# Kernel tuning notes

Measured on AMD Instinct MI355X. Metric: run time of the kernel, lower is better.

Reference implementation:

```python
import jax, jax.numpy as jnp
import numpy as np

N = 6144
INPUT_SIZE = 1024
HIDDEN = 256
NEG_INF = -9e15  # matches torch masked_fill value -9000000000000000.0


def setup_inputs() -> dict:
    key = jax.random.key(0)
    k1, k2, k3, k4 = jax.random.split(key, 4)
    nodes_embed = jax.random.normal(k1, (N, INPUT_SIZE), dtype=jnp.float32)
    node_adj = jax.random.randint(k2, (N, N), 0, 2, dtype=jnp.int32)
    # learned params (xavier-uniform-ish scaling)
    limW = np.sqrt(6.0 / (INPUT_SIZE + HIDDEN))
    W = jax.random.uniform(k3, (INPUT_SIZE, HIDDEN), minval=-limW, maxval=limW, dtype=jnp.float32)
    lima = 1.414 * np.sqrt(6.0 / (2 * HIDDEN + 1))
    a_edge = jax.random.uniform(k4, (2 * HIDDEN,), minval=-lima, maxval=lima, dtype=jnp.float32)
    return {"nodes_embed": nodes_embed, "W": W, "a_edge": a_edge, "node_adj": node_adj}


def reference(nodes_embed, W, a_edge, node_adj):
    # h = nodes_embed @ W : [N, hidden]
    h = nodes_embed @ W
    # W_edge([h_i ; h_j]) decomposes exactly: (h_i @ a1) + (h_j @ a2)
    a1, a2 = a_edge[:HIDDEN], a_edge[HIDDEN:]
    score = (h @ a1)[:, None] + (h @ a2)[None, :]  # [N, N]
    adj_f = node_adj.astype(h.dtype)
    weight = jax.nn.leaky_relu(adj_f * score, negative_slope=0.2)
    weight = jnp.where(node_adj == 0, jnp.asarray(NEG_INF, h.dtype), weight)
    attention = jax.nn.softmax(weight, axis=-1)
    # dropout in eval mode (identity)
    return attention @ h  # [N, hidden]
```

## Files before the change

kernel.cpp:

```cpp
#include <hip/hip_runtime.h>
#include <hip/hip_bf16.h>

#define NN 6144
#define INPUT 1024
#define HID 256

using frag  = __attribute__((ext_vector_type(8))) short;
using f32x4 = __attribute__((ext_vector_type(4))) float;

static __device__ __forceinline__ unsigned short bf16u(float x) {
    unsigned u = __float_as_uint(x);
    u += 0x7fff + ((u >> 16) & 1);
    return (unsigned short)(u >> 16);
}

static __device__ __forceinline__ void gll16nt(const void* g, void* l) {
    __builtin_amdgcn_global_load_lds((__attribute__((address_space(1))) const void*)g,
                                     (__attribute__((address_space(3))) void*)l, 16, 0, 2);
}

static __device__ __forceinline__ void lds_barrier() {
    asm volatile("s_waitcnt lgkmcnt(0)" ::: "memory");
    __builtin_amdgcn_s_barrier();
    __builtin_amdgcn_sched_barrier(0);
}


__global__ __launch_bounds__(256) void k_prep(const float* __restrict__ X,
                                              const float* __restrict__ W,
                                              unsigned short* __restrict__ Xbp,
                                              unsigned short* __restrict__ Wtp) {
    int b = blockIdx.x;
    if (b < 3072) {
        int t = b * 256 + threadIdx.x;
        int i = t >> 7, k8 = t & 127;
        const float4* p = reinterpret_cast<const float4*>(X + (size_t)i * INPUT + k8 * 8);
        float4 x0 = p[0], x1 = p[1];
        frag v;
        v[0] = (short)bf16u(x0.x); v[1] = (short)bf16u(x0.y);
        v[2] = (short)bf16u(x0.z); v[3] = (short)bf16u(x0.w);
        v[4] = (short)bf16u(x1.x); v[5] = (short)bf16u(x1.y);
        v[6] = (short)bf16u(x1.z); v[7] = (short)bf16u(x1.w);
        size_t off = ((size_t)((i >> 4) * 32 + (k8 >> 2))) * 512 + (k8 & 3) * 128 + (i & 15) * 8;
        *reinterpret_cast<frag*>(Xbp + off) = v;
    } else {
        int u = (b - 3072) * 256 + threadIdx.x;
        int n = u >> 7, k8 = u & 127;
        int k = k8 * 8;
        frag v;
#pragma unroll
        for (int e = 0; e < 8; e++) v[e] = (short)bf16u(W[(size_t)(k + e) * HID + n]);
        size_t off = ((size_t)((n >> 4) * 32 + (k8 >> 2))) * 512 + (k8 & 3) * 128 + (n & 15) * 8;
        *reinterpret_cast<frag*>(Wtp + off) = v;
    }
}

__global__ __launch_bounds__(256, 4) void k_gemm1(const unsigned short* __restrict__ Xbp,
                                                  const unsigned short* __restrict__ Wtp,
                                                  const float* __restrict__ a_edge,
                                                  unsigned short* __restrict__ hTp,
                                                  float* __restrict__ s1,
                                                  float* __restrict__ s2) {
    int t = threadIdx.x;
    int w = t >> 6, l = t & 63, lm = l & 15, q = l >> 4;
    int bx = blockIdx.x, by = blockIdx.y;
    int i0 = bx * 32;
    int tn = by * 4 + w;

    const unsigned short* pA0 = Xbp + (size_t)(bx * 2) * 32 * 512 + l * 8;
    const unsigned short* pA1 = Xbp + (size_t)(bx * 2 + 1) * 32 * 512 + l * 8;
    const unsigned short* pB  = Wtp + (size_t)tn * 32 * 512 + l * 8;

    f32x4 acc0 = {}, acc1 = {};
    frag a0s[3], a1s[3], bs[3];
#pragma unroll
    for (int s = 0; s < 2; s++) {
        a0s[s] = *reinterpret_cast<const frag*>(pA0 + s * 512);
        a1s[s] = *reinterpret_cast<const frag*>(pA1 + s * 512);
        bs[s]  = *reinterpret_cast<const frag*>(pB  + s * 512);
    }
#pragma unroll
    for (int tk = 0; tk < 32; tk++) {
        int cur = tk % 3;
        if (tk < 30) {
            int nx = (tk + 2) % 3;
            a0s[nx] = *reinterpret_cast<const frag*>(pA0 + (tk + 2) * 512);
            a1s[nx] = *reinterpret_cast<const frag*>(pA1 + (tk + 2) * 512);
            bs[nx]  = *reinterpret_cast<const frag*>(pB  + (tk + 2) * 512);
        }
        acc0 = __builtin_amdgcn_mfma_f32_16x16x32_bf16(a0s[cur], bs[cur], acc0, 0, 0, 0);
        acc1 = __builtin_amdgcn_mfma_f32_16x16x32_bf16(a1s[cur], bs[cur], acc1, 0, 0, 0);
    }

    unsigned short* tb = hTp + ((size_t)bx * 16 + tn) * 512;
    ushort4 o;
    o.x = bf16u(acc0[0]); o.y = bf16u(acc0[1]); o.z = bf16u(acc0[2]); o.w = bf16u(acc0[3]);
    *reinterpret_cast<ushort4*>(tb + (q >> 1) * 128 + lm * 8 + (q & 1) * 4) = o;
    o.x = bf16u(acc1[0]); o.y = bf16u(acc1[1]); o.z = bf16u(acc1[2]); o.w = bf16u(acc1[3]);
    *reinterpret_cast<ushort4*>(tb + (2 + (q >> 1)) * 128 + lm * 8 + (q & 1) * 4) = o;

    float a1v = a_edge[tn * 16 + lm], a2v = a_edge[HID + tn * 16 + lm];
#pragma unroll
    for (int h = 0; h < 2; h++) {
        const f32x4& ac = h ? acc1 : acc0;
#pragma unroll
        for (int r = 0; r < 4; r++) {
            float v1 = ac[r] * a1v, v2 = ac[r] * a2v;
            v1 += __shfl_xor(v1, 1); v2 += __shfl_xor(v2, 1);
            v1 += __shfl_xor(v1, 2); v2 += __shfl_xor(v2, 2);
            v1 += __shfl_xor(v1, 4); v2 += __shfl_xor(v2, 4);
            v1 += __shfl_xor(v1, 8); v2 += __shfl_xor(v2, 8);
            if (lm == 0) {
                atomicAdd(&s1[i0 + h * 16 + q * 4 + r], v1);
                atomicAdd(&s2[i0 + h * 16 + q * 4 + r], v2);
            }
        }
    }
}

__global__ __launch_bounds__(512, 2) void k_attn(const int* __restrict__ adj,
                                                 const float* __restrict__ s1,
                                                 const float* __restrict__ s2,
                                                 const unsigned short* __restrict__ hTp,
                                                 float* __restrict__ U4,
                                                 float* __restrict__ denom4) {
    __shared__ unsigned short P[2][32][136];
    __shared__ int adjS[2][32][128];
    int t = threadIdx.x;
    int m = t >> 4, cg = t & 15;
    int i0 = blockIdx.x * 32;
    int q4 = blockIdx.y, j0 = q4 * 1536;
    int w = t >> 6, l = t & 63, lm = l & 15, q = l >> 4;

    float s1v = s1[i0 + m];
    const int* astage = adj + (size_t)(i0 + w * 4 + (l >> 5)) * NN + j0 + (l & 31) * 4;
    const float* s2p = s2 + j0 + cg * 8;

    const unsigned short* hb = hTp + (size_t)(w * 2) * 512 + l * 8;
    int tjb = q4 * 48;

    f32x4 acc[2][2] = {};
    float dsum = 0.f;

    gll16nt(astage, &adjS[0][w * 4][0]);
    gll16nt(astage + 2 * NN, &adjS[0][w * 4 + 2][0]);

    for (int c = 0; c < 12; c++) {
        int buf = c & 1, jc = c * 128;

        float4 sv0 = *reinterpret_cast<const float4*>(s2p + jc);
        float4 sv1 = *reinterpret_cast<const float4*>(s2p + jc + 4);

        frag bf[8];
#pragma unroll
        for (int kk = 0; kk < 4; kk++)
#pragma unroll
            for (int nt = 0; nt < 2; nt++)
                bf[kk * 2 + nt] = *reinterpret_cast<const frag*>(
                    hb + ((size_t)(tjb + c * 4 + kk) * 16 + nt) * 512);

        int jn = (c < 11) ? jc + 128 : jc;
        gll16nt(astage + jn, &adjS[buf ^ 1][w * 4][0]);
        gll16nt(astage + jn + 2 * NN, &adjS[buf ^ 1][w * 4 + 2][0]);

        asm volatile("s_waitcnt vmcnt(12)" ::: "memory");
        __builtin_amdgcn_sched_barrier(0);

        {
            const int* aL = &adjS[buf][m][cg * 8];
            int4 av0 = *reinterpret_cast<const int4*>(aL);
            int4 av1 = *reinterpret_cast<const int4*>(aL + 4);
            float sc, wv, p0, p1, p2, p3, p4, p5, p6, p7;
            sc = s1v + sv0.x; wv = fmaxf(sc, 0.2f * sc); p0 = av0.x ? __expf(wv) : 0.f;
            sc = s1v + sv0.y; wv = fmaxf(sc, 0.2f * sc); p1 = av0.y ? __expf(wv) : 0.f;
            sc = s1v + sv0.z; wv = fmaxf(sc, 0.2f * sc); p2 = av0.z ? __expf(wv) : 0.f;
            sc = s1v + sv0.w; wv = fmaxf(sc, 0.2f * sc); p3 = av0.w ? __expf(wv) : 0.f;
            sc = s1v + sv1.x; wv = fmaxf(sc, 0.2f * sc); p4 = av1.x ? __expf(wv) : 0.f;
            sc = s1v + sv1.y; wv = fmaxf(sc, 0.2f * sc); p5 = av1.y ? __expf(wv) : 0.f;
            sc = s1v + sv1.z; wv = fmaxf(sc, 0.2f * sc); p6 = av1.z ? __expf(wv) : 0.f;
            sc = s1v + sv1.w; wv = fmaxf(sc, 0.2f * sc); p7 = av1.w ? __expf(wv) : 0.f;
            dsum += ((p0 + p1) + (p2 + p3)) + ((p4 + p5) + (p6 + p7));
            frag pk;
            pk[0] = (short)bf16u(p0); pk[1] = (short)bf16u(p1);
            pk[2] = (short)bf16u(p2); pk[3] = (short)bf16u(p3);
            pk[4] = (short)bf16u(p4); pk[5] = (short)bf16u(p5);
            pk[6] = (short)bf16u(p6); pk[7] = (short)bf16u(p7);
            *reinterpret_cast<frag*>(&P[buf][m][cg * 8]) = pk;
        }

        lds_barrier();

        __builtin_amdgcn_s_setprio(1);
#pragma unroll
        for (int kk = 0; kk < 4; kk++) {
            frag a0 = *reinterpret_cast<const frag*>(&P[buf][lm][kk * 32 + q * 8]);
            frag a1 = *reinterpret_cast<const frag*>(&P[buf][16 + lm][kk * 32 + q * 8]);
#pragma unroll
            for (int nt = 0; nt < 2; nt++) {
                acc[0][nt] = __builtin_amdgcn_mfma_f32_16x16x32_bf16(a0, bf[kk * 2 + nt], acc[0][nt], 0, 0, 0);
                acc[1][nt] = __builtin_amdgcn_mfma_f32_16x16x32_bf16(a1, bf[kk * 2 + nt], acc[1][nt], 0, 0, 0);
            }
        }
        __builtin_amdgcn_s_setprio(0);
    }

    float v = dsum;
    v += __shfl_xor(v, 1); v += __shfl_xor(v, 2);
    v += __shfl_xor(v, 4); v += __shfl_xor(v, 8);
    if (cg == 0) denom4[(size_t)q4 * NN + i0 + m] = v;

    float* Ub = U4 + (size_t)q4 * NN * HID;
#pragma unroll
    for (int h = 0; h < 2; h++)
#pragma unroll
        for (int nt = 0; nt < 2; nt++)
#pragma unroll
            for (int r = 0; r < 4; r++)
                Ub[(size_t)(i0 + h * 16 + q * 4 + r) * HID + w * 32 + nt * 16 + lm] = acc[h][nt][r];
}

__global__ __launch_bounds__(256) void k_norm(const float* __restrict__ U4,
                                              const float* __restrict__ denom4,
                                              float* __restrict__ out) {
    int i = blockIdx.x, t = threadIdx.x;
    size_t S = (size_t)NN * HID;
    size_t base = (size_t)i * HID + t;
    float u = U4[base] + U4[base + S] + U4[base + 2 * S] + U4[base + 3 * S];
    float d = denom4[i] + denom4[i + NN] + denom4[i + 2 * NN] + denom4[i + 3 * NN];
    out[base] = (d != 0.f) ? u / d : 0.f;
}

extern "C" void kernel_launch(void* const* d_in, const int* in_sizes, int n_in,
                              void* d_out, int out_size, void* d_ws, size_t ws_size,
                              hipStream_t stream) {
    const float* X      = (const float*)d_in[0];
    const float* W      = (const float*)d_in[1];
    const float* a_edge = (const float*)d_in[2];
    const int*   adj    = (const int*)d_in[3];
    float* out = (float*)d_out;

    float* U4     = (float*)d_ws;
    float* denom4 = U4 + (size_t)4 * NN * HID;
    float* s1     = denom4 + (size_t)4 * NN;
    float* s2     = s1 + NN;
    unsigned short* hTp = (unsigned short*)(s2 + NN);
    unsigned short* Wtp = hTp + (size_t)HID * NN;
    unsigned short* Xbp = (unsigned short*)U4;

    hipMemsetAsync(s1, 0, 2 * NN * sizeof(float), stream);
    k_prep<<<3072 + 128, 256, 0, stream>>>(X, W, Xbp, Wtp);
    k_gemm1<<<dim3(NN / 32, 4), 256, 0, stream>>>(Xbp, Wtp, a_edge, hTp, s1, s2);
    k_attn<<<dim3(NN / 32, 4), 512, 0, stream>>>(adj, s1, s2, hTp, U4, denom4);
    k_norm<<<NN, 256, 0, stream>>>(U4, denom4, out);
}
```

Measured before the change: 296.9 us.

## Retile attention kernel to 64-row blocks with 8-way column split

The attention kernel now processes 64 rows per block over 768-column slices (8 splits instead of 4), with 64-column chunks. Each hT fragment loaded from global memory is reused across four row tiles instead of two, which halves B-operand traffic per output. The adjacency prefetch is issued after the wait instead of before, and the non-temporal cache hint is dropped. The cost is twice as many partial U buffers to write and reduce in the normalization kernel, plus a larger workspace.

Measured after the change: 306.4 us. +3.2%, slower.

```diff
diff --git a/kernel.cpp b/kernel.cpp
--- a/kernel.cpp
+++ b/kernel.cpp
@@ -14,9 +14,9 @@
     return (unsigned short)(u >> 16);
 }
 
-static __device__ __forceinline__ void gll16nt(const void* g, void* l) {
+static __device__ __forceinline__ void gll16(const void* g, void* l) {
     __builtin_amdgcn_global_load_lds((__attribute__((address_space(1))) const void*)g,
-                                     (__attribute__((address_space(3))) void*)l, 16, 0, 2);
+                                     (__attribute__((address_space(3))) void*)l, 16, 0, 0);
 }
 
 static __device__ __forceinline__ void lds_barrier() {
@@ -122,49 +122,47 @@
                                                  const float* __restrict__ s1,
                                                  const float* __restrict__ s2,
                                                  const unsigned short* __restrict__ hTp,
-                                                 float* __restrict__ U4,
-                                                 float* __restrict__ denom4) {
-    __shared__ unsigned short P[2][32][136];
-    __shared__ int adjS[2][32][128];
+                                                 float* __restrict__ U8,
+                                                 float* __restrict__ denom8) {
+    __shared__ unsigned short P[2][64][72];
+    __shared__ int adjS[2][64][64];
     int t = threadIdx.x;
-    int m = t >> 4, cg = t & 15;
-    int i0 = blockIdx.x * 32;
-    int q4 = blockIdx.y, j0 = q4 * 1536;
+    int m = t >> 3, cg = t & 7;
+    int i0 = blockIdx.x * 64;
+    int q8 = blockIdx.y, j0 = q8 * 768;
     int w = t >> 6, l = t & 63, lm = l & 15, q = l >> 4;
 
     float s1v = s1[i0 + m];
-    const int* astage = adj + (size_t)(i0 + w * 4 + (l >> 5)) * NN + j0 + (l & 31) * 4;
+    const int* astage = adj + (size_t)(i0 + w * 8 + (l >> 4)) * NN + j0 + (l & 15) * 4;
     const float* s2p = s2 + j0 + cg * 8;
 
-    const unsigned short* hb = hTp + (size_t)(w * 2) * 512 + l * 8;
-    int tjb = q4 * 48;
-
-    f32x4 acc[2][2] = {};
+    const unsigned short* hb = hTp + ((size_t)(q8 * 24) * 16 + w * 2) * 512 + l * 8;
+
+    f32x4 acc[4][2] = {};
     float dsum = 0.f;
 
-    gll16nt(astage, &adjS[0][w * 4][0]);
-    gll16nt(astage + 2 * NN, &adjS[0][w * 4 + 2][0]);
+#define STAGE(JC, BUF) { \
+        gll16(astage + (JC), &adjS[BUF][w * 8][0]); \
+        gll16(astage + (JC) + 4 * NN, &adjS[BUF][w * 8 + 4][0]); }
+
+    STAGE(0, 0)
 
     for (int c = 0; c < 12; c++) {
-        int buf = c & 1, jc = c * 128;
-
+        int buf = c & 1, jc = c * 64;
+
+        frag bf[4];
+#pragma unroll
+        for (int kk = 0; kk < 2; kk++)
+#pragma unroll
+            for (int nt = 0; nt < 2; nt++)
+                bf[kk * 2 + nt] = *reinterpret_cast<const frag*>(
+                    hb + ((size_t)(c * 2 + kk) * 16 + nt) * 512);
         float4 sv0 = *reinterpret_cast<const float4*>(s2p + jc);
         float4 sv1 = *reinterpret_cast<const float4*>(s2p + jc + 4);
 
-        frag bf[8];
-#pragma unroll
-        for (int kk = 0; kk < 4; kk++)
-#pragma unroll
-            for (int nt = 0; nt < 2; nt++)
-                bf[kk * 2 + nt] = *reinterpret_cast<const frag*>(
-                    hb + ((size_t)(tjb + c * 4 + kk) * 16 + nt) * 512);
-
-        int jn = (c < 11) ? jc + 128 : jc;
-        gll16nt(astage + jn, &adjS[buf ^ 1][w * 4][0]);
-        gll16nt(astage + jn + 2 * NN, &adjS[buf ^ 1][w * 4 + 2][0]);
-
-        asm volatile("s_waitcnt vmcnt(12)" ::: "memory");
+        asm volatile("s_waitcnt vmcnt(6)" ::: "memory");
         __builtin_amdgcn_sched_barrier(0);
+        if (c < 11) STAGE(jc + 64, buf ^ 1)
 
         {
             const int* aL = &adjS[buf][m][cg * 8];
@@ -192,26 +190,30 @@
 
         __builtin_amdgcn_s_setprio(1);
 #pragma unroll
-        for (int kk = 0; kk < 4; kk++) {
+        for (int kk = 0; kk < 2; kk++) {
             frag a0 = *reinterpret_cast<const frag*>(&P[buf][lm][kk * 32 + q * 8]);
             frag a1 = *reinterpret_cast<const frag*>(&P[buf][16 + lm][kk * 32 + q * 8]);
+            frag a2 = *reinterpret_cast<const frag*>(&P[buf][32 + lm][kk * 32 + q * 8]);
+            frag a3 = *reinterpret_cast<const frag*>(&P[buf][48 + lm][kk * 32 + q * 8]);
 #pragma unroll
             for (int nt = 0; nt < 2; nt++) {
                 acc[0][nt] = __builtin_amdgcn_mfma_f32_16x16x32_bf16(a0, bf[kk * 2 + nt], acc[0][nt], 0, 0, 0);
                 acc[1][nt] = __builtin_amdgcn_mfma_f32_16x16x32_bf16(a1, bf[kk * 2 + nt], acc[1][nt], 0, 0, 0);
+                acc[2][nt] = __builtin_amdgcn_mfma_f32_16x16x32_bf16(a2, bf[kk * 2 + nt], acc[2][nt], 0, 0, 0);
+                acc[3][nt] = __builtin_amdgcn_mfma_f32_16x16x32_bf16(a3, bf[kk * 2 + nt], acc[3][nt], 0, 0, 0);
             }
         }
         __builtin_amdgcn_s_setprio(0);
     }
+#undef STAGE
 
     float v = dsum;
-    v += __shfl_xor(v, 1); v += __shfl_xor(v, 2);
-    v += __shfl_xor(v, 4); v += __shfl_xor(v, 8);
-    if (cg == 0) denom4[(size_t)q4 * NN + i0 + m] = v;
-
-    float* Ub = U4 + (size_t)q4 * NN * HID;
-#pragma unroll
-    for (int h = 0; h < 2; h++)
+    v += __shfl_xor(v, 1); v += __shfl_xor(v, 2); v += __shfl_xor(v, 4);
+    if (cg == 0) denom8[(size_t)q8 * NN + i0 + m] = v;
+
+    float* Ub = U8 + (size_t)q8 * NN * HID;
+#pragma unroll
+    for (int h = 0; h < 4; h++)
 #pragma unroll
         for (int nt = 0; nt < 2; nt++)
 #pragma unroll
@@ -219,14 +221,18 @@
                 Ub[(size_t)(i0 + h * 16 + q * 4 + r) * HID + w * 32 + nt * 16 + lm] = acc[h][nt][r];
 }
 
-__global__ __launch_bounds__(256) void k_norm(const float* __restrict__ U4,
-                                              const float* __restrict__ denom4,
+__global__ __launch_bounds__(256) void k_norm(const float* __restrict__ U8,
+                                              const float* __restrict__ denom8,
                                               float* __restrict__ out) {
     int i = blockIdx.x, t = threadIdx.x;
     size_t S = (size_t)NN * HID;
     size_t base = (size_t)i * HID + t;
-    float u = U4[base] + U4[base + S] + U4[base + 2 * S] + U4[base + 3 * S];
-    float d = denom4[i] + denom4[i + NN] + denom4[i + 2 * NN] + denom4[i + 3 * NN];
+    float u = 0.f, d = 0.f;
+#pragma unroll
+    for (int s = 0; s < 8; s++) {
+        u += U8[base + s * S];
+        d += denom8[i + s * NN];
+    }
     out[base] = (d != 0.f) ? u / d : 0.f;
 }
 
@@ -239,17 +245,17 @@
     const int*   adj    = (const int*)d_in[3];
     float* out = (float*)d_out;
 
-    float* U4     = (float*)d_ws;
-    float* denom4 = U4 + (size_t)4 * NN * HID;
-    float* s1     = denom4 + (size_t)4 * NN;
+    float* U8     = (float*)d_ws;
+    float* denom8 = U8 + (size_t)8 * NN * HID;
+    float* s1     = denom8 + (size_t)8 * NN;
     float* s2     = s1 + NN;
     unsigned short* hTp = (unsigned short*)(s2 + NN);
     unsigned short* Wtp = hTp + (size_t)HID * NN;
-    unsigned short* Xbp = (unsigned short*)U4;
+    unsigned short* Xbp = (unsigned short*)U8;
 
     hipMemsetAsync(s1, 0, 2 * NN * sizeof(float), stream);
     k_prep<<<3072 + 128, 256, 0, stream>>>(X, W, Xbp, Wtp);
     k_gemm1<<<dim3(NN / 32, 4), 256, 0, stream>>>(Xbp, Wtp, a_edge, hTp, s1, s2);
-    k_attn<<<dim3(NN / 32, 4), 512, 0, stream>>>(adj, s1, s2, hTp, U4, denom4);
-    k_norm<<<NN, 256, 0, stream>>>(U4, denom4, out);
-}
+    k_attn<<<dim3(NN / 64, 8), 512, 0, stream>>>(adj, s1, s2, hTp, U8, denom8);
+    k_norm<<<NN, 256, 0, stream>>>(U8, denom8, out);
+}
```
